# Optimization experiments

Measured on AMD Instinct MI355X. Metric: run time of the kernel, lower is better.

Reference implementation:

```python
import math
import jax, jax.numpy as jnp
import numpy as np

D_MODEL = 256
NUM_FEATURES = 512  # 2 * d_model (module default)
BATCH, SEQ = 4, 4096
EPS = 1e-6
INPUT_SCALE = 0.25  # keeps exp(xW/sqrt(d) - ||x||^2/2) numerically meaningful


def _make_projection(key):
    # Orthogonal random features: ceil(M/d)=2 QR blocks, then sqrt(|gauss|) row scaling.
    k1, k2, k3 = jax.random.split(key, 3)
    q1, _ = jnp.linalg.qr(jax.random.normal(k1, (D_MODEL, D_MODEL), jnp.float32))
    q2, _ = jnp.linalg.qr(jax.random.normal(k2, (D_MODEL, D_MODEL), jnp.float32))
    proj = jnp.concatenate([q1, q2], axis=1)[:, :NUM_FEATURES]  # (d, M)
    scaling = jnp.sqrt(jnp.abs(jax.random.normal(k3, (D_MODEL, 1), jnp.float32)))
    return proj * scaling


def setup_inputs() -> dict:
    key = jax.random.key(0)
    kq, kk, kv, kp = jax.random.split(key, 4)
    shape = (BATCH, SEQ, D_MODEL)
    return {
        "query": jax.random.normal(kq, shape, jnp.float32) * INPUT_SCALE,
        "key": jax.random.normal(kk, shape, jnp.float32) * INPUT_SCALE,
        "value": jax.random.normal(kv, shape, jnp.float32) * INPUT_SCALE,
        "projection": _make_projection(kp),  # (d_model, num_features) buffer
    }


def _phi(x, projection):
    # phi(x) = exp(xW/sqrt(d) - ||x||^2/2) / sqrt(M)
    d = x.shape[-1]
    m = projection.shape[-1]
    proj = jnp.matmul(x, projection) / math.sqrt(d)  # (B, L, M)
    sq = 0.5 * jnp.sum(x * x, axis=-1, keepdims=True)  # (B, L, 1)
    return jnp.exp(proj - sq) / math.sqrt(m)


def reference(query, key, value, projection):
    qp = _phi(query, projection)  # (B, L, M)
    kp = _phi(key, projection)    # (B, L, M)
    B, L, M = qp.shape
    D = value.shape[-1]

    # Causal linear attention: running KV-state scan, O(B*M*D) state
    # (same math as cumsum of k' (outer) v, without materializing (B,L,M,D)).
    def step(carry, inp):
        kv_state, k_state = carry  # (B,M,D), (B,M)
        q_t, k_t, v_t = inp        # (B,M), (B,M), (B,D)
        kv_state = kv_state + k_t[:, :, None] * v_t[:, None, :]
        k_state = k_state + k_t
        num = jnp.einsum('bm,bmd->bd', q_t, kv_state)
        den = jnp.einsum('bm,bm->b', q_t, k_state)[:, None] + EPS
        return (kv_state, k_state), num / den

    init = (jnp.zeros((B, M, D), qp.dtype), jnp.zeros((B, M), qp.dtype))
    xs = (jnp.swapaxes(qp, 0, 1), jnp.swapaxes(kp, 0, 1), jnp.swapaxes(value, 0, 1))
    _, out = jax.lax.scan(step, init, xs)  # (L, B, D)
    return jnp.swapaxes(out, 0, 1)  # (B, L, D)
```

## Files before the change

### kernel.cpp

```cpp
#include <hip/hip_runtime.h>

#define B_ 4
#define L_ 4096
#define D_ 256
#define M_ 512
#define C_ 256
#define NC_ 16
#define NG_ (B_*NC_)
#define EPS_ 1e-6f
#define RSQRT_D_ 0.0625f
#define RSQRT_M_ 0.044194173824159216f

typedef __attribute__((ext_vector_type(8))) short short8;
typedef __attribute__((ext_vector_type(4))) short short4v;
typedef __attribute__((ext_vector_type(4))) float floatx4;

__device__ __forceinline__ short f2b(float f) {
  union { float f; unsigned u; } c; c.f = f;
  unsigned r = c.u + 0x7fffu + ((c.u >> 16) & 1u);
  return (short)(r >> 16);
}
__device__ __forceinline__ float b2f(short s) {
  union { unsigned u; float f; } c; c.u = ((unsigned)(unsigned short)s) << 16;
  return c.f;
}

#define OFF_SB   0u
#define OFF_WT   16777216u
#define OFF_QP   17039360u
#define OFF_KP   33816576u
#define OFF_KPT  50593792u
#define OFF_VT   67371008u
#define OFF_AM   75759616u
#define OFF_PB   84148224u
#define OFF_ZP   100925440u

__device__ __forceinline__ void mfma_tile_gemm(
    const short* __restrict__ Ag, int lda,
    const short* __restrict__ Bg, int ldb,
    int K, short* sA, short* sB, floatx4 acc[4][4])
{
  const int tid  = threadIdx.x;
  const int lane = tid & 63;
  const int wave = tid >> 6;
  const int wm = wave >> 1, wn = wave & 1;
  const int q = lane >> 4, ml = lane & 15;

  short8 pa[4], pb[4];
  #pragma unroll
  for (int it = 0; it < 4; ++it) {
    int ci = tid + 256 * it;
    int m = ci >> 3, k8 = ci & 7;
    pa[it] = *(const short8*)(Ag + (size_t)m * lda + k8 * 8);
    pb[it] = *(const short8*)(Bg + (size_t)m * ldb + k8 * 8);
  }
  for (int k0 = 0; k0 < K; k0 += 64) {
    #pragma unroll
    for (int it = 0; it < 4; ++it) {
      int ci = tid + 256 * it;
      int m = ci >> 3, k8 = ci & 7;
      int dst = (k8 >> 2) * 512 + (m >> 4) * 64 + (k8 & 3) * 16 + ((m & 15) ^ k8);
      *(short8*)(sA + dst * 8) = pa[it];
      *(short8*)(sB + dst * 8) = pb[it];
    }
    if (k0 + 64 < K) {
      #pragma unroll
      for (int it = 0; it < 4; ++it) {
        int ci = tid + 256 * it;
        int m = ci >> 3, k8 = ci & 7;
        pa[it] = *(const short8*)(Ag + (size_t)m * lda + k0 + 64 + k8 * 8);
        pb[it] = *(const short8*)(Bg + (size_t)m * ldb + k0 + 64 + k8 * 8);
      }
    }
    __syncthreads();
    #pragma unroll
    for (int ks = 0; ks < 2; ++ks) {
      short8 a[4], b[4];
      int k8 = ks * 4 + q;
      #pragma unroll
      for (int i = 0; i < 4; ++i) {
        int ca = ks * 512 + (wm * 4 + i) * 64 + q * 16 + (ml ^ k8);
        a[i] = *(const short8*)(sA + ca * 8);
        int cb = ks * 512 + (wn * 4 + i) * 64 + q * 16 + (ml ^ k8);
        b[i] = *(const short8*)(sB + cb * 8);
      }
      #pragma unroll
      for (int i = 0; i < 4; ++i)
        #pragma unroll
        for (int j = 0; j < 4; ++j)
          acc[i][j] = __builtin_amdgcn_mfma_f32_16x16x32_bf16(a[i], b[j], acc[i][j], 0, 0, 0);
    }
    __syncthreads();
  }
}

__global__ __launch_bounds__(256) void transpose_cvt_kernel(
    const float* __restrict__ v, const float* __restrict__ W,
    short* __restrict__ vT, short* __restrict__ Wt)
{
  const int z = blockIdx.z;
  const float* src; short* dst; int ld_in, ld_out;
  if (z < NG_) {
    if (blockIdx.x >= 4) return;
    src = v + (size_t)z * (C_*D_) + (size_t)blockIdx.y * 64 * D_ + blockIdx.x * 64;
    dst = vT + (size_t)z * (D_*C_) + (size_t)blockIdx.x * 64 * C_ + blockIdx.y * 64;
    ld_in = D_; ld_out = C_;
  } else {
    src = W + (size_t)blockIdx.y * 64 * M_ + blockIdx.x * 64;
    dst = Wt + (size_t)blockIdx.x * 64 * D_ + blockIdx.y * 64;
    ld_in = M_; ld_out = D_;
  }
  __shared__ short sm[64 * 65];
  const int tid = threadIdx.x;
  #pragma unroll
  for (int it = 0; it < 4; ++it) {
    int ci = tid + 256 * it;
    int row = ci >> 4, c4 = ci & 15;
    float4 x = *(const float4*)(src + (size_t)row * ld_in + c4 * 4);
    sm[(c4 * 4 + 0) * 65 + row] = f2b(x.x);
    sm[(c4 * 4 + 1) * 65 + row] = f2b(x.y);
    sm[(c4 * 4 + 2) * 65 + row] = f2b(x.z);
    sm[(c4 * 4 + 3) * 65 + row] = f2b(x.w);
  }
  __syncthreads();
  #pragma unroll
  for (int it = 0; it < 2; ++it) {
    int ci = tid + 256 * it;
    int dr = ci >> 3, t8 = ci & 7;
    short8 o;
    #pragma unroll
    for (int u = 0; u < 8; ++u) o[u] = sm[dr * 65 + t8 * 8 + u];
    *(short8*)(dst + (size_t)dr * ld_out + t8 * 8) = o;
  }
}

__global__ __launch_bounds__(512) void phi_mfma_kernel(
    const float* __restrict__ qin, const float* __restrict__ kin,
    const short* __restrict__ Wt,
    short* __restrict__ qp, short* __restrict__ kp, short* __restrict__ kpT,
    float* __restrict__ ZP)
{
  const bool is_k = (blockIdx.z == 1);
  const float* X = is_k ? kin : qin;
  short* outP = is_k ? kp : qp;
  const int idl = blockIdx.x + 2 * blockIdx.y;
  const int row0 = ((idl & 7) + 8 * (idl >> 4)) * 128;
  const int col0 = ((idl >> 3) & 1) * 256;
  __shared__ short smem[34816];
  __shared__ float zsb[512];
  __shared__ float sqs[128];
  short* sA = smem;
  short* sB = smem + 8192;
  const int tid = threadIdx.x, lane = tid & 63, wave = tid >> 6;
  const int wm = wave >> 2, wn = wave & 3, q = lane >> 4, ml = lane & 15;
  const int c8 = tid & 7, r8 = tid >> 3;
  floatx4 acc[4][4];
  #pragma unroll
  for (int i = 0; i < 4; ++i)
    #pragma unroll
    for (int j = 0; j < 4; ++j) acc[i][j] = (floatx4){0.f,0.f,0.f,0.f};

  float4 px0[2], px1[2];
  #pragma unroll
  for (int it = 0; it < 2; ++it) {
    const float* src = X + (size_t)(row0 + r8 + 64 * it) * D_ + c8 * 8;
    px0[it] = *(const float4*)src;
    px1[it] = *(const float4*)(src + 4);
  }
  float ssq[2] = {0.f, 0.f};
  for (int k0 = 0; k0 < D_; k0 += 64) {
    #pragma unroll
    for (int it = 0; it < 2; ++it) {
      int m = r8 + 64 * it;
      float4 x0 = px0[it], x1 = px1[it];
      short8 vv;
      vv[0] = f2b(x0.x); vv[1] = f2b(x0.y); vv[2] = f2b(x0.z); vv[3] = f2b(x0.w);
      vv[4] = f2b(x1.x); vv[5] = f2b(x1.y); vv[6] = f2b(x1.z); vv[7] = f2b(x1.w);
      ssq[it] += x0.x*x0.x + x0.y*x0.y + x0.z*x0.z + x0.w*x0.w
               + x1.x*x1.x + x1.y*x1.y + x1.z*x1.z + x1.w*x1.w;
      *(short8*)(sA + (c8 * 128 + (m ^ c8)) * 8) = vv;
    }
    #pragma unroll
    for (int it = 0; it < 4; ++it) {
      int mm = r8 + 64 * it;
      short8 wb = *(const short8*)(Wt + (size_t)(col0 + mm) * D_ + k0 + c8 * 8);
      *(short8*)(sB + (c8 * 256 + (mm ^ c8)) * 8) = wb;
    }
    if (k0 + 64 < D_) {
      #pragma unroll
      for (int it = 0; it < 2; ++it) {
        const float* src = X + (size_t)(row0 + r8 + 64 * it) * D_ + k0 + 64 + c8 * 8;
        px0[it] = *(const float4*)src;
        px1[it] = *(const float4*)(src + 4);
      }
    }
    __syncthreads();
    #pragma unroll
    for (int ks = 0; ks < 2; ++ks) {
      short8 a[4], b[4];
      int kk = ks * 4 + q;
      #pragma unroll
      for (int i = 0; i < 4; ++i) {
        int ra = (wm * 64 + i * 16 + ml) ^ kk;
        a[i] = *(const short8*)(sA + (kk * 128 + ra) * 8);
        int rb = (wn * 64 + i * 16 + ml) ^ kk;
        b[i] = *(const short8*)(sB + (kk * 256 + rb) * 8);
      }
      #pragma unroll
      for (int i = 0; i < 4; ++i)
        #pragma unroll
        for (int j = 0; j < 4; ++j)
          acc[i][j] = __builtin_amdgcn_mfma_f32_16x16x32_bf16(a[i], b[j], acc[i][j], 0, 0, 0);
    }
    __syncthreads();
  }
  #pragma unroll
  for (int o = 1; o < 8; o <<= 1)
    #pragma unroll
    for (int it = 0; it < 2; ++it) ssq[it] += __shfl_xor(ssq[it], o);
  if (c8 == 0) {
    sqs[r8] = 0.5f * ssq[0];
    sqs[r8 + 64] = 0.5f * ssq[1];
  }
  __syncthreads();

  if (!is_k) {
    #pragma unroll
    for (int i = 0; i < 4; ++i) {
      int rl = wm * 64 + i * 16 + q * 4;
      float sqv[4];
      #pragma unroll
      for (int r = 0; r < 4; ++r) sqv[r] = sqs[rl + r];
      #pragma unroll
      for (int j = 0; j < 4; ++j) {
        int cl = wn * 64 + j * 16 + ml;
        #pragma unroll
        for (int r = 0; r < 4; ++r) {
          float pv = __expf(fmaf(acc[i][j][r], RSQRT_D_, -sqv[r])) * RSQRT_M_;
          smem[(size_t)(rl + r) * 264 + cl] = f2b(pv);
        }
      }
    }
    __syncthreads();
    #pragma unroll
    for (int it = 0; it < 8; ++it) {
      int idx = tid + 512 * it;
      int row = idx >> 5, cc8 = idx & 31;
      short8 vv = *(const short8*)(smem + (size_t)row * 264 + cc8 * 8);
      *(short8*)(outP + (size_t)(row0 + row) * M_ + col0 + cc8 * 8) = vv;
    }
  } else {
    float csum[4] = {0.f, 0.f, 0.f, 0.f};
    #pragma unroll
    for (int i = 0; i < 4; ++i) {
      int rl = wm * 64 + i * 16 + q * 4;
      float sqv[4];
      #pragma unroll
      for (int r = 0; r < 4; ++r) sqv[r] = sqs[rl + r];
      #pragma unroll
      for (int j = 0; j < 4; ++j) {
        int cl = wn * 64 + j * 16 + ml;
        short4v tb;
        #pragma unroll
        for (int r = 0; r < 4; ++r) {
          float pv = __expf(fmaf(acc[i][j][r], RSQRT_D_, -sqv[r])) * RSQRT_M_;
          short bv = f2b(pv);
          outP[(size_t)(row0 + rl + r) * M_ + col0 + cl] = bv;
          tb[r] = bv;
          csum[j] += b2f(bv);
        }
        *(short4v*)(smem + (size_t)cl * 136 + rl) = tb;
      }
    }
    #pragma unroll
    for (int j = 0; j < 4; ++j) {
      csum[j] += __shfl_xor(csum[j], 16);
      csum[j] += __shfl_xor(csum[j], 32);
    }
    if (lane < 16) {
      #pragma unroll
      for (int j = 0; j < 4; ++j)
        zsb[wm * 256 + wn * 64 + j * 16 + ml] = csum[j];
    }
    __syncthreads();
    int g = row0 >> 8, tb0 = row0 & 255;
    #pragma unroll
    for (int it = 0; it < 8; ++it) {
      int ci = tid + 512 * it;
      int t8 = ci & 15, cc = ci >> 4;
      short8 vv = *(const short8*)(smem + (size_t)cc * 136 + t8 * 8);
      *(short8*)(kpT + (size_t)g * (M_*C_) + (size_t)(col0 + cc) * C_ + tb0 + t8 * 8) = vv;
    }
    if (tid < 256) {
      float s = zsb[tid] + zsb[256 + tid];
      int p = (row0 >> 7) & 1;
      ZP[((size_t)g * 2 + p) * M_ + col0 + tid] = s;
    }
  }
}

__global__ __launch_bounds__(256) void mega_kernel(
    const short* __restrict__ vT, const short* __restrict__ kpT,
    const short* __restrict__ qp, const short* __restrict__ kp,
    short* __restrict__ Sb, short* __restrict__ Am)
{
  const int id = blockIdx.x + 4 * blockIdx.y + 12 * blockIdx.z;
  const int t12 = id >> 3;
  const int g  = (id & 7) + 8 * (t12 / 12);
  const int inner = t12 % 12;
  const int bx = inner & 3, by = inner >> 2;
  __shared__ short smem[17408];
  const int tid = threadIdx.x;

  floatx4 acc[4][4];
  #pragma unroll
  for (int i = 0; i < 4; ++i)
    #pragma unroll
    for (int j = 0; j < 4; ++j) acc[i][j] = (floatx4){0.f,0.f,0.f,0.f};
  const int lane = tid & 63, wave = tid >> 6;
  const int wm = wave >> 1, wn = wave & 1, q = lane >> 4, ln = lane & 15;

  if (by < 2) {
    const int m0 = bx * 128, d0 = by * 128;
    mfma_tile_gemm(vT + (size_t)g * (D_*C_) + (size_t)d0 * C_, C_,
                   kpT + (size_t)g * (M_*C_) + (size_t)m0 * C_, C_, C_,
                   smem, smem + 8192, acc);
    #pragma unroll
    for (int i = 0; i < 4; ++i) {
      int lr = wm * 64 + i * 16 + q * 4;
      #pragma unroll
      for (int j = 0; j < 4; ++j) {
        int lc = wn * 64 + j * 16 + ln;
        #pragma unroll
        for (int r = 0; r < 4; ++r)
          smem[(size_t)(lr + r) * 136 + lc] = f2b(acc[i][j][r]);
      }
    }
    __syncthreads();
    #pragma unroll
    for (int it = 0; it < 8; ++it) {
      int idx = tid + 256 * it;
      int row = idx >> 4, c8 = idx & 15;
      short8 vv = *(const short8*)(smem + (size_t)row * 136 + c8 * 8);
      *(short8*)(Sb + ((size_t)g * D_ + d0 + row) * M_ + m0 + c8 * 8) = vv;
    }
  } else {
    const int tt0 = (bx >> 1) * 128, tp0 = (bx & 1) * 128;
    short* Ag = Am + (size_t)g * (C_*C_);
    if (tp0 > tt0) {
      short8 z8 = 0;
      #pragma unroll
      for (int it = 0; it < 8; ++it) {
        int ci = tid + 256 * it;
        int row = ci >> 4, c8 = ci & 15;
        *(short8*)(Ag + (size_t)(tt0 + row) * C_ + tp0 + c8 * 8) = z8;
      }
      return;
    }
    const size_t cb = (size_t)g * C_;
    mfma_tile_gemm(qp + (cb + tt0) * M_, M_, kp + (cb + tp0) * M_, M_, M_,
                   smem, smem + 8192, acc);
    #pragma unroll
    for (int i = 0; i < 4; ++i) {
      int lr = wm * 64 + i * 16 + q * 4;
      #pragma unroll
      for (int j = 0; j < 4; ++j) {
        int lc = wn * 64 + j * 16 + ln;
        #pragma unroll
        for (int r = 0; r < 4; ++r) {
          short bv = ((tp0 + lc) <= (tt0 + lr + r)) ? f2b(acc[i][j][r]) : (short)0;
          smem[(size_t)(lr + r) * 136 + lc] = bv;
        }
      }
    }
    __syncthreads();
    #pragma unroll
    for (int it = 0; it < 8; ++it) {
      int idx = tid + 256 * it;
      int row = idx >> 4, c8 = idx & 15;
      short8 vv = *(const short8*)(smem + (size_t)row * 136 + c8 * 8);
      *(short8*)(Ag + (size_t)(tt0 + row) * C_ + tp0 + c8 * 8) = vv;
    }
  }
}

__global__ __launch_bounds__(256) void prefixS_kernel(
    const short* __restrict__ Sb, short* __restrict__ Pb)
{
  int j = blockIdx.x * 256 + threadIdx.x;
  int b = j >> 14, e8 = j & 16383;
  size_t base = ((size_t)b * NC_) * 131072 + (size_t)e8 * 8;
  short8 t[NC_];
  #pragma unroll
  for (int i = 0; i < NC_; ++i)
    t[i] = *(const short8*)(Sb + base + (size_t)i * 131072);
  float run[8] = {0.f,0.f,0.f,0.f,0.f,0.f,0.f,0.f};
  #pragma unroll
  for (int i = 0; i < NC_; ++i) {
    short8 o;
    #pragma unroll
    for (int u = 0; u < 8; ++u) { o[u] = f2b(run[u]); run[u] += b2f(t[i][u]); }
    *(short8*)(Pb + base + (size_t)i * 131072) = o;
  }
}

__global__ __launch_bounds__(256) void out_mfma_kernel(
    const short* __restrict__ qp, const short* __restrict__ Pb,
    const short* __restrict__ Am, const short* __restrict__ vT,
    const float* __restrict__ ZP, float* __restrict__ out)
{
  const int id = blockIdx.x + 2 * blockIdx.y + 8 * blockIdx.z;
  const int g  = (id & 7) + 8 * (id >> 6);
  const int inner = (id >> 3) & 7;
  const int d0 = (inner & 1) * 128, tt0 = (inner >> 1) * 64;
  __shared__ short smem[16896];
  __shared__ float zbuf[512];
  __shared__ float dbuf[64];
  short* sA = smem; short* sB = smem + 4096;
  const int tid = threadIdx.x, lane = tid & 63, wave = tid >> 6;
  const int wm = wave >> 1, wn = wave & 1, q = lane >> 4, ml = lane & 15;
  const int r8 = tid >> 3;

  {
    int b = g >> 4, gi = g & 15;
    float s0 = 0.f, s1 = 0.f;
    const float* zp0 = ZP + (size_t)(b * NC_) * 2 * M_;
    for (int i = 0; i < gi; ++i) {
      const float* r = zp0 + (size_t)i * 2 * M_;
      s0 += r[tid] + r[M_ + tid];
      s1 += r[tid + 256] + r[M_ + tid + 256];
    }
    zbuf[tid] = s0; zbuf[tid + 256] = s1;
    if (tid < 64) dbuf[tid] = 0.f;
  }
  __syncthreads();

  floatx4 acc[2][4];
  #pragma unroll
  for (int i = 0; i < 2; ++i)
    #pragma unroll
    for (int j = 0; j < 4; ++j) acc[i][j] = (floatx4){0.f,0.f,0.f,0.f};

  {
    const short* Ag = qp + ((size_t)g * C_ + tt0) * M_;
    const short* Bg = Pb + (size_t)g * (D_*M_) + (size_t)d0 * M_;
    float dp[2] = {0.f, 0.f};
    short8 pa[2], pb[4];
    #pragma unroll
    for (int it = 0; it < 2; ++it) {
      int ci = tid + 256 * it;
      int m = ci >> 3, k8 = ci & 7;
      pa[it] = *(const short8*)(Ag + (size_t)m * M_ + k8 * 8);
    }
    #pragma unroll
    for (int it = 0; it < 4; ++it) {
      int ci = tid + 256 * it;
      int m = ci >> 3, k8 = ci & 7;
      pb[it] = *(const short8*)(Bg + (size_t)m * M_ + k8 * 8);
    }
    for (int k0 = 0; k0 < M_; k0 += 64) {
      #pragma unroll
      for (int it = 0; it < 2; ++it) {
        int ci = tid + 256 * it;
        int m = ci >> 3, k8 = ci & 7;
        int dst = (k8 >> 2) * 256 + (m >> 4) * 64 + (k8 & 3) * 16 + ((m & 15) ^ k8);
        *(short8*)(sA + dst * 8) = pa[it];
        const float* zz = zbuf + k0 + k8 * 8;
        float d = 0.f;
        #pragma unroll
        for (int u = 0; u < 8; ++u) d = fmaf(b2f(pa[it][u]), zz[u], d);
        dp[it] += d;
      }
      #pragma unroll
      for (int it = 0; it < 4; ++it) {
        int ci = tid + 256 * it;
        int m = ci >> 3, k8 = ci & 7;
        int dst = (k8 >> 2) * 512 + (m >> 4) * 64 + (k8 & 3) * 16 + ((m & 15) ^ k8);
        *(short8*)(sB + dst * 8) = pb[it];
      }
      if (k0 + 64 < M_) {
        #pragma unroll
        for (int it = 0; it < 2; ++it) {
          int ci = tid + 256 * it;
          int m = ci >> 3, k8 = ci & 7;
          pa[it] = *(const short8*)(Ag + (size_t)m * M_ + k0 + 64 + k8 * 8);
        }
        #pragma unroll
        for (int it = 0; it < 4; ++it) {
          int ci = tid + 256 * it;
          int m = ci >> 3, k8 = ci & 7;
          pb[it] = *(const short8*)(Bg + (size_t)m * M_ + k0 + 64 + k8 * 8);
        }
      }
      __syncthreads();
      #pragma unroll
      for (int ks = 0; ks < 2; ++ks) {
        short8 a[2], b[4];
        int k8 = ks * 4 + q;
        #pragma unroll
        for (int i = 0; i < 2; ++i) {
          int ca = ks * 256 + (wm * 2 + i) * 64 + q * 16 + (ml ^ k8);
          a[i] = *(const short8*)(sA + ca * 8);
        }
        #pragma unroll
        for (int j = 0; j < 4; ++j) {
          int cb = ks * 512 + (wn * 4 + j) * 64 + q * 16 + (ml ^ k8);
          b[j] = *(const short8*)(sB + cb * 8);
        }
        #pragma unroll
        for (int i = 0; i < 2; ++i)
          #pragma unroll
          for (int j = 0; j < 4; ++j)
            acc[i][j] = __builtin_amdgcn_mfma_f32_16x16x32_bf16(a[i], b[j], acc[i][j], 0, 0, 0);
      }
      __syncthreads();
    }
    #pragma unroll
    for (int o = 1; o < 8; o <<= 1)
      #pragma unroll
      for (int it = 0; it < 2; ++it) dp[it] += __shfl_xor(dp[it], o);
    if ((tid & 7) == 0) {
      #pragma unroll
      for (int it = 0; it < 2; ++it) dbuf[r8 + 32 * it] += dp[it];
    }
  }

  {
    const short* Ag = Am + ((size_t)g * C_ + tt0) * C_;
    const short* Bg = vT + (size_t)g * (D_*C_) + (size_t)d0 * C_;
    float dp[2] = {0.f, 0.f};
    short8 pa[2], pb[4];
    #pragma unroll
    for (int it = 0; it < 2; ++it) {
      int ci = tid + 256 * it;
      int m = ci >> 3, k8 = ci & 7;
      pa[it] = *(const short8*)(Ag + (size_t)m * C_ + k8 * 8);
    }
    #pragma unroll
    for (int it = 0; it < 4; ++it) {
      int ci = tid + 256 * it;
      int m = ci >> 3, k8 = ci & 7;
      pb[it] = *(const short8*)(Bg + (size_t)m * C_ + k8 * 8);
    }
    for (int k0 = 0; k0 < C_; k0 += 64) {
      #pragma unroll
      for (int it = 0; it < 2; ++it) {
        int ci = tid + 256 * it;
        int m = ci >> 3, k8 = ci & 7;
        int dst = (k8 >> 2) * 256 + (m >> 4) * 64 + (k8 & 3) * 16 + ((m & 15) ^ k8);
        *(short8*)(sA + dst * 8) = pa[it];
        float d = 0.f;
        #pragma unroll
        for (int u = 0; u < 8; ++u) d += b2f(pa[it][u]);
        dp[it] += d;
      }
      #pragma unroll
      for (int it = 0; it < 4; ++it) {
        int ci = tid + 256 * it;
        int m = ci >> 3, k8 = ci & 7;
        int dst = (k8 >> 2) * 512 + (m >> 4) * 64 + (k8 & 3) * 16 + ((m & 15) ^ k8);
        *(short8*)(sB + dst * 8) = pb[it];
      }
      if (k0 + 64 < C_) {
        #pragma unroll
        for (int it = 0; it < 2; ++it) {
          int ci = tid + 256 * it;
          int m = ci >> 3, k8 = ci & 7;
          pa[it] = *(const short8*)(Ag + (size_t)m * C_ + k0 + 64 + k8 * 8);
        }
        #pragma unroll
        for (int it = 0; it < 4; ++it) {
          int ci = tid + 256 * it;
          int m = ci >> 3, k8 = ci & 7;
          pb[it] = *(const short8*)(Bg + (size_t)m * C_ + k0 + 64 + k8 * 8);
        }
      }
      __syncthreads();
      #pragma unroll
      for (int ks = 0; ks < 2; ++ks) {
        short8 a[2], b[4];
        int k8 = ks * 4 + q;
        #pragma unroll
        for (int i = 0; i < 2; ++i) {
          int ca = ks * 256 + (wm * 2 + i) * 64 + q * 16 + (ml ^ k8);
          a[i] = *(const short8*)(sA + ca * 8);
        }
        #pragma unroll
        for (int j = 0; j < 4; ++j) {
          int cb = ks * 512 + (wn * 4 + j) * 64 + q * 16 + (ml ^ k8);
          b[j] = *(const short8*)(sB + cb * 8);
        }
        #pragma unroll
        for (int i = 0; i < 2; ++i)
          #pragma unroll
          for (int j = 0; j < 4; ++j)
            acc[i][j] = __builtin_amdgcn_mfma_f32_16x16x32_bf16(a[i], b[j], acc[i][j], 0, 0, 0);
      }
      __syncthreads();
    }
    #pragma unroll
    for (int o = 1; o < 8; o <<= 1)
      #pragma unroll
      for (int it = 0; it < 2; ++it) dp[it] += __shfl_xor(dp[it], o);
    if ((tid & 7) == 0) {
      #pragma unroll
      for (int it = 0; it < 2; ++it) dbuf[r8 + 32 * it] += dp[it];
    }
  }
  __syncthreads();

  float* smF = (float*)smem;
  #pragma unroll
  for (int i = 0; i < 2; ++i) {
    int lr = wm * 32 + i * 16 + q * 4;
    #pragma unroll
    for (int r = 0; r < 4; ++r) {
      float rc = 1.0f / (dbuf[lr + r] + EPS_);
      #pragma unroll
      for (int j = 0; j < 4; ++j) {
        int lc = wn * 64 + j * 16 + ml;
        smF[(size_t)(lr + r) * 132 + lc] = acc[i][j][r] * rc;
      }
    }
  }
  __syncthreads();
  #pragma unroll
  for (int it = 0; it < 8; ++it) {
    int idx = tid + 256 * it;
    int row = idx >> 5, c4 = idx & 31;
    float4 val = *(const float4*)(smF + (size_t)row * 132 + c4 * 4);
    *(float4*)(out + (size_t)(g * C_ + tt0 + row) * D_ + d0 + c4 * 4) = val;
  }
}

extern "C" void kernel_launch(void* const* d_in, const int* in_sizes, int n_in,
                              void* d_out, int out_size, void* d_ws, size_t ws_size,
                              hipStream_t stream) {
  const float* q = (const float*)d_in[0];
  const float* k = (const float*)d_in[1];
  const float* v = (const float*)d_in[2];
  const float* W = (const float*)d_in[3];
  float* out = (float*)d_out;
  char* ws = (char*)d_ws;

  short* Sb  = (short*)(ws + OFF_SB);
  short* Wt  = (short*)(ws + OFF_WT);
  short* qp  = (short*)(ws + OFF_QP);
  short* kp  = (short*)(ws + OFF_KP);
  short* kpT = (short*)(ws + OFF_KPT);
  short* vT  = (short*)(ws + OFF_VT);
  short* Am  = (short*)(ws + OFF_AM);
  short* Pb  = (short*)(ws + OFF_PB);
  float* ZP  = (float*)(ws + OFF_ZP);

  transpose_cvt_kernel<<<dim3(8, 4, NG_ + 1), 256, 0, stream>>>(v, W, vT, Wt);
  phi_mfma_kernel<<<dim3(2, 128, 2), 512, 0, stream>>>(q, k, Wt, qp, kp, kpT, ZP);
  mega_kernel<<<dim3(4, 3, NG_), 256, 0, stream>>>(vT, kpT, qp, kp, Sb, Am);
  prefixS_kernel<<<(B_*D_*M_)/2048, 256, 0, stream>>>(Sb, Pb);
  out_mfma_kernel<<<dim3(2, 4, NG_), 256, 0, stream>>>(qp, Pb, Am, vT, ZP, out);
}
```

Measured before the change: 156.5 us.

## Stage GEMM tiles with direct global-to-LDS async loads instead of register prefetch

Replaces the register-staged prefetch (global load to VGPRs, then LDS store) in several GEMM loops with global_load_lds 16-byte direct copies. Per-thread source addresses are permuted so that the contiguous LDS destination reproduces the existing XOR-swizzled layout. This removes the VGPR staging and the LDS write instructions, but also drops the software prefetch overlap: each k-step now issues its loads and waits at a barrier before computing. The row-sum and dot-product side computations now reread the A tile from LDS.

```diff
diff --git a/kernel.cpp b/kernel.cpp
--- a/kernel.cpp
+++ b/kernel.cpp
@@ -25,6 +25,12 @@
   return c.f;
 }
 
+__device__ __forceinline__ void async_copy16(const short* g, short* l) {
+  __builtin_amdgcn_global_load_lds(
+      (const __attribute__((address_space(1))) void*)(g),
+      (__attribute__((address_space(3))) void*)(l), 16, 0, 0);
+}
+
 #define OFF_SB   0u
 #define OFF_WT   16777216u
 #define OFF_QP   17039360u
@@ -46,31 +52,21 @@
   const int wm = wave >> 1, wn = wave & 1;
   const int q = lane >> 4, ml = lane & 15;
 
-  short8 pa[4], pb[4];
+  int mloc[4], koff[4];
   #pragma unroll
   for (int it = 0; it < 4; ++it) {
-    int ci = tid + 256 * it;
-    int m = ci >> 3, k8 = ci & 7;
-    pa[it] = *(const short8*)(Ag + (size_t)m * lda + k8 * 8);
-    pb[it] = *(const short8*)(Bg + (size_t)m * ldb + k8 * 8);
+    int s = tid + 256 * it;
+    int x = s & 15, l = (s >> 4) & 3, M = (s >> 6) & 7, h = s >> 9;
+    int k8 = 4 * h + l;
+    mloc[it] = M * 16 + (x ^ k8);
+    koff[it] = k8 * 8;
   }
   for (int k0 = 0; k0 < K; k0 += 64) {
     #pragma unroll
     for (int it = 0; it < 4; ++it) {
-      int ci = tid + 256 * it;
-      int m = ci >> 3, k8 = ci & 7;
-      int dst = (k8 >> 2) * 512 + (m >> 4) * 64 + (k8 & 3) * 16 + ((m & 15) ^ k8);
-      *(short8*)(sA + dst * 8) = pa[it];
-      *(short8*)(sB + dst * 8) = pb[it];
-    }
-    if (k0 + 64 < K) {
-      #pragma unroll
-      for (int it = 0; it < 4; ++it) {
-        int ci = tid + 256 * it;
-        int m = ci >> 3, k8 = ci & 7;
-        pa[it] = *(const short8*)(Ag + (size_t)m * lda + k0 + 64 + k8 * 8);
-        pb[it] = *(const short8*)(Bg + (size_t)m * ldb + k0 + 64 + k8 * 8);
-      }
+      int s = tid + 256 * it;
+      async_copy16(Ag + (size_t)mloc[it] * lda + k0 + koff[it], sA + s * 8);
+      async_copy16(Bg + (size_t)mloc[it] * ldb + k0 + koff[it], sB + s * 8);
     }
     __syncthreads();
     #pragma unroll
@@ -160,6 +156,15 @@
     #pragma unroll
     for (int j = 0; j < 4; ++j) acc[i][j] = (floatx4){0.f,0.f,0.f,0.f};
 
+  int wmm[4], wc8[4];
+  #pragma unroll
+  for (int it = 0; it < 4; ++it) {
+    int s = tid + 512 * it;
+    int cc = s >> 8;
+    wmm[it] = (s & 255) ^ cc;
+    wc8[it] = cc;
+  }
+
   float4 px0[2], px1[2];
   #pragma unroll
   for (int it = 0; it < 2; ++it) {
@@ -169,6 +174,11 @@
   }
   float ssq[2] = {0.f, 0.f};
   for (int k0 = 0; k0 < D_; k0 += 64) {
+    #pragma unroll
+    for (int it = 0; it < 4; ++it) {
+      int s = tid + 512 * it;
+      async_copy16(Wt + (size_t)(col0 + wmm[it]) * D_ + k0 + wc8[it] * 8, sB + s * 8);
+    }
     #pragma unroll
     for (int it = 0; it < 2; ++it) {
       int m = r8 + 64 * it;
@@ -179,12 +189,6 @@
       ssq[it] += x0.x*x0.x + x0.y*x0.y + x0.z*x0.z + x0.w*x0.w
                + x1.x*x1.x + x1.y*x1.y + x1.z*x1.z + x1.w*x1.w;
       *(short8*)(sA + (c8 * 128 + (m ^ c8)) * 8) = vv;
-    }
-    #pragma unroll
-    for (int it = 0; it < 4; ++it) {
-      int mm = r8 + 64 * it;
-      short8 wb = *(const short8*)(Wt + (size_t)(col0 + mm) * D_ + k0 + c8 * 8);
-      *(short8*)(sB + (c8 * 256 + (mm ^ c8)) * 8) = wb;
     }
     if (k0 + 64 < D_) {
       #pragma unroll
@@ -435,6 +439,22 @@
   }
   __syncthreads();
 
+  int mA[2], kA[2], mB[4], kB[4];
+  #pragma unroll
+  for (int it = 0; it < 2; ++it) {
+    int s = tid + 256 * it;
+    int x = s & 15, l = (s >> 4) & 3, M = (s >> 6) & 3, h = s >> 8;
+    int k8 = 4 * h + l;
+    mA[it] = M * 16 + (x ^ k8); kA[it] = k8 * 8;
+  }
+  #pragma unroll
+  for (int it = 0; it < 4; ++it) {
+    int s = tid + 256 * it;
+    int x = s & 15, l = (s >> 4) & 3, M = (s >> 6) & 7, h = s >> 9;
+    int k8 = 4 * h + l;
+    mB[it] = M * 16 + (x ^ k8); kB[it] = k8 * 8;
+  }
+
   floatx4 acc[2][4];
   #pragma unroll
   for (int i = 0; i < 2; ++i)
@@ -445,54 +465,26 @@
     const short* Ag = qp + ((size_t)g * C_ + tt0) * M_;
     const short* Bg = Pb + (size_t)g * (D_*M_) + (size_t)d0 * M_;
     float dp[2] = {0.f, 0.f};
-    short8 pa[2], pb[4];
-    #pragma unroll
-    for (int it = 0; it < 2; ++it) {
-      int ci = tid + 256 * it;
-      int m = ci >> 3, k8 = ci & 7;
-      pa[it] = *(const short8*)(Ag + (size_t)m * M_ + k8 * 8);
-    }
-    #pragma unroll
-    for (int it = 0; it < 4; ++it) {
-      int ci = tid + 256 * it;
-      int m = ci >> 3, k8 = ci & 7;
-      pb[it] = *(const short8*)(Bg + (size_t)m * M_ + k8 * 8);
-    }
     for (int k0 = 0; k0 < M_; k0 += 64) {
+      #pragma unroll
+      for (int it = 0; it < 2; ++it)
+        async_copy16(Ag + (size_t)mA[it] * M_ + k0 + kA[it], sA + (tid + 256 * it) * 8);
+      #pragma unroll
+      for (int it = 0; it < 4; ++it)
+        async_copy16(Bg + (size_t)mB[it] * M_ + k0 + kB[it], sB + (tid + 256 * it) * 8);
+      __syncthreads();
       #pragma unroll
       for (int it = 0; it < 2; ++it) {
         int ci = tid + 256 * it;
         int m = ci >> 3, k8 = ci & 7;
         int dst = (k8 >> 2) * 256 + (m >> 4) * 64 + (k8 & 3) * 16 + ((m & 15) ^ k8);
-        *(short8*)(sA + dst * 8) = pa[it];
+        short8 pa = *(const short8*)(sA + dst * 8);
         const float* zz = zbuf + k0 + k8 * 8;
         float d = 0.f;
         #pragma unroll
-        for (int u = 0; u < 8; ++u) d = fmaf(b2f(pa[it][u]), zz[u], d);
+        for (int u = 0; u < 8; ++u) d = fmaf(b2f(pa[u]), zz[u], d);
         dp[it] += d;
       }
-      #pragma unroll
-      for (int it = 0; it < 4; ++it) {
-        int ci = tid + 256 * it;
-        int m = ci >> 3, k8 = ci & 7;
-        int dst = (k8 >> 2) * 512 + (m >> 4) * 64 + (k8 & 3) * 16 + ((m & 15) ^ k8);
-        *(short8*)(sB + dst * 8) = pb[it];
-      }
-      if (k0 + 64 < M_) {
-        #pragma unroll
-        for (int it = 0; it < 2; ++it) {
-          int ci = tid + 256 * it;
-          int m = ci >> 3, k8 = ci & 7;
-          pa[it] = *(const short8*)(Ag + (size_t)m * M_ + k0 + 64 + k8 * 8);
-        }
-        #pragma unroll
-        for (int it = 0; it < 4; ++it) {
-          int ci = tid + 256 * it;
-          int m = ci >> 3, k8 = ci & 7;
-          pb[it] = *(const short8*)(Bg + (size_t)m * M_ + k0 + 64 + k8 * 8);
-        }
-      }
-      __syncthreads();
       #pragma unroll
       for (int ks = 0; ks < 2; ++ks) {
         short8 a[2], b[4];
@@ -529,53 +521,25 @@
     const short* Ag = Am + ((size_t)g * C_ + tt0) * C_;
     const short* Bg = vT + (size_t)g * (D_*C_) + (size_t)d0 * C_;
     float dp[2] = {0.f, 0.f};
-    short8 pa[2], pb[4];
-    #pragma unroll
-    for (int it = 0; it < 2; ++it) {
-      int ci = tid + 256 * it;
-      int m = ci >> 3, k8 = ci & 7;
-      pa[it] = *(const short8*)(Ag + (size_t)m * C_ + k8 * 8);
-    }
-    #pragma unroll
-    for (int it = 0; it < 4; ++it) {
-      int ci = tid + 256 * it;
-      int m = ci >> 3, k8 = ci & 7;
-      pb[it] = *(const short8*)(Bg + (size_t)m * C_ + k8 * 8);
-    }
     for (int k0 = 0; k0 < C_; k0 += 64) {
+      #pragma unroll
+      for (int it = 0; it < 2; ++it)
+        async_copy16(Ag + (size_t)mA[it] * C_ + k0 + kA[it], sA + (tid + 256 * it) * 8);
+      #pragma unroll
+      for (int it = 0; it < 4; ++it)
+        async_copy16(Bg + (size_t)mB[it] * C_ + k0 + kB[it], sB + (tid + 256 * it) * 8);
+      __syncthreads();
       #pragma unroll
       for (int it = 0; it < 2; ++it) {
         int ci = tid + 256 * it;
         int m = ci >> 3, k8 = ci & 7;
         int dst = (k8 >> 2) * 256 + (m >> 4) * 64 + (k8 & 3) * 16 + ((m & 15) ^ k8);
-        *(short8*)(sA + dst * 8) = pa[it];
+        short8 pa = *(const short8*)(sA + dst * 8);
         float d = 0.f;
         #pragma unroll
-        for (int u = 0; u < 8; ++u) d += b2f(pa[it][u]);
+        for (int u = 0; u < 8; ++u) d += b2f(pa[u]);
         dp[it] += d;
       }
-      #pragma unroll
-      for (int it = 0; it < 4; ++it) {
-        int ci = tid + 256 * it;
-        int m = ci >> 3, k8 = ci & 7;
-        int dst = (k8 >> 2) * 512 + (m >> 4) * 64 + (k8 & 3) * 16 + ((m & 15) ^ k8);
-        *(short8*)(sB + dst * 8) = pb[it];
-      }
-      if (k0 + 64 < C_) {
-        #pragma unroll
-        for (int it = 0; it < 2; ++it) {
-          int ci = tid + 256 * it;
-          int m = ci >> 3, k8 = ci & 7;
-          pa[it] = *(const short8*)(Ag + (size_t)m * C_ + k0 + 64 + k8 * 8);
-        }
-        #pragma unroll
-        for (int it = 0; it < 4; ++it) {
-          int ci = tid + 256 * it;
-          int m = ci >> 3, k8 = ci & 7;
-          pb[it] = *(const short8*)(Bg + (size_t)m * C_ + k0 + 64 + k8 * 8);
-        }
-      }
-      __syncthreads();
       #pragma unroll
       for (int ks = 0; ks < 2; ++ks) {
         short8 a[2], b[4];
```

Measured after the change: 175.6 us. 12.2% more time.

## Use direct global-to-LDS async loads in tile GEMM and precompute z prefix sums

Applied to the files above, without the earlier changes.

The shared MFMA tile GEMM now stages A/B tiles with global_load_lds direct-to-LDS copies in an unswizzled layout, replacing the register-staged prefetch and XOR-swizzled stores. Separately, the per-chunk prefix sum of key-feature totals (ZP) is computed once by extra blocks in prefixS_kernel into ZPX, which reuses the Wt workspace slot. out_mfma_kernel then reads that instead of looping over previous chunks. The GEMM change drops the prefetch overlap and swizzle, so it risks LDS bank conflicts and exposed load latency, and the Wt region must no longer be needed by the time prefixS runs.

```diff
diff --git a/kernel.cpp b/kernel.cpp
--- a/kernel.cpp
+++ b/kernel.cpp
@@ -25,6 +25,12 @@
   return c.f;
 }
 
+__device__ __forceinline__ void async_copy16(const short* g, short* l) {
+  __builtin_amdgcn_global_load_lds(
+      (const __attribute__((address_space(1))) void*)(g),
+      (__attribute__((address_space(3))) void*)(l), 16, 0, 0);
+}
+
 #define OFF_SB   0u
 #define OFF_WT   16777216u
 #define OFF_QP   17039360u
@@ -46,31 +52,13 @@
   const int wm = wave >> 1, wn = wave & 1;
   const int q = lane >> 4, ml = lane & 15;
 
-  short8 pa[4], pb[4];
-  #pragma unroll
-  for (int it = 0; it < 4; ++it) {
-    int ci = tid + 256 * it;
-    int m = ci >> 3, k8 = ci & 7;
-    pa[it] = *(const short8*)(Ag + (size_t)m * lda + k8 * 8);
-    pb[it] = *(const short8*)(Bg + (size_t)m * ldb + k8 * 8);
-  }
   for (int k0 = 0; k0 < K; k0 += 64) {
     #pragma unroll
     for (int it = 0; it < 4; ++it) {
-      int ci = tid + 256 * it;
-      int m = ci >> 3, k8 = ci & 7;
-      int dst = (k8 >> 2) * 512 + (m >> 4) * 64 + (k8 & 3) * 16 + ((m & 15) ^ k8);
-      *(short8*)(sA + dst * 8) = pa[it];
-      *(short8*)(sB + dst * 8) = pb[it];
-    }
-    if (k0 + 64 < K) {
-      #pragma unroll
-      for (int it = 0; it < 4; ++it) {
-        int ci = tid + 256 * it;
-        int m = ci >> 3, k8 = ci & 7;
-        pa[it] = *(const short8*)(Ag + (size_t)m * lda + k0 + 64 + k8 * 8);
-        pb[it] = *(const short8*)(Bg + (size_t)m * ldb + k0 + 64 + k8 * 8);
-      }
+      int s = tid + 256 * it;
+      int m = s >> 3, k8 = s & 7;
+      async_copy16(Ag + (size_t)m * lda + k0 + k8 * 8, sA + s * 8);
+      async_copy16(Bg + (size_t)m * ldb + k0 + k8 * 8, sB + s * 8);
     }
     __syncthreads();
     #pragma unroll
@@ -79,10 +67,10 @@
       int k8 = ks * 4 + q;
       #pragma unroll
       for (int i = 0; i < 4; ++i) {
-        int ca = ks * 512 + (wm * 4 + i) * 64 + q * 16 + (ml ^ k8);
-        a[i] = *(const short8*)(sA + ca * 8);
-        int cb = ks * 512 + (wn * 4 + i) * 64 + q * 16 + (ml ^ k8);
-        b[i] = *(const short8*)(sB + cb * 8);
+        int ra = wm * 64 + i * 16 + ml;
+        a[i] = *(const short8*)(sA + (ra * 8 + k8) * 8);
+        int rb = wn * 64 + i * 16 + ml;
+        b[i] = *(const short8*)(sB + (rb * 8 + k8) * 8);
       }
       #pragma unroll
       for (int i = 0; i < 4; ++i)
@@ -385,8 +373,21 @@
 }
 
 __global__ __launch_bounds__(256) void prefixS_kernel(
-    const short* __restrict__ Sb, short* __restrict__ Pb)
+    const short* __restrict__ Sb, short* __restrict__ Pb,
+    const float* __restrict__ ZP, float* __restrict__ ZPX)
 {
+  if (blockIdx.x >= 256) {
+    int idx = (blockIdx.x - 256) * 256 + threadIdx.x;
+    int b = idx >> 9, m = idx & 511;
+    float run = 0.f;
+    #pragma unroll
+    for (int i = 0; i < NC_; ++i) {
+      int g = b * NC_ + i;
+      ZPX[(size_t)g * M_ + m] = run;
+      run += ZP[((size_t)g * 2 + 0) * M_ + m] + ZP[((size_t)g * 2 + 1) * M_ + m];
+    }
+    return;
+  }
   int j = blockIdx.x * 256 + threadIdx.x;
   int b = j >> 14, e8 = j & 16383;
   size_t base = ((size_t)b * NC_) * 131072 + (size_t)e8 * 8;
@@ -407,7 +408,7 @@
 __global__ __launch_bounds__(256) void out_mfma_kernel(
     const short* __restrict__ qp, const short* __restrict__ Pb,
     const short* __restrict__ Am, const short* __restrict__ vT,
-    const float* __restrict__ ZP, float* __restrict__ out)
+    const float* __restrict__ ZPX, float* __restrict__ out)
 {
   const int id = blockIdx.x + 2 * blockIdx.y + 8 * blockIdx.z;
   const int g  = (id & 7) + 8 * (id >> 6);
@@ -422,15 +423,8 @@
   const int r8 = tid >> 3;
 
   {
-    int b = g >> 4, gi = g & 15;
-    float s0 = 0.f, s1 = 0.f;
-    const float* zp0 = ZP + (size_t)(b * NC_) * 2 * M_;
-    for (int i = 0; i < gi; ++i) {
-      const float* r = zp0 + (size_t)i * 2 * M_;
-      s0 += r[tid] + r[M_ + tid];
-      s1 += r[tid + 256] + r[M_ + tid + 256];
-    }
-    zbuf[tid] = s0; zbuf[tid + 256] = s1;
+    zbuf[tid]       = ZPX[(size_t)g * M_ + tid];
+    zbuf[tid + 256] = ZPX[(size_t)g * M_ + 256 + tid];
     if (tid < 64) dbuf[tid] = 0.f;
   }
   __syncthreads();
@@ -652,10 +646,11 @@
   short* Am  = (short*)(ws + OFF_AM);
   short* Pb  = (short*)(ws + OFF_PB);
   float* ZP  = (float*)(ws + OFF_ZP);
+  float* ZPX = (float*)(ws + OFF_WT);
 
   transpose_cvt_kernel<<<dim3(8, 4, NG_ + 1), 256, 0, stream>>>(v, W, vT, Wt);
   phi_mfma_kernel<<<dim3(2, 128, 2), 512, 0, stream>>>(q, k, Wt, qp, kp, kpT, ZP);
   mega_kernel<<<dim3(4, 3, NG_), 256, 0, stream>>>(vT, kpT, qp, kp, Sb, Am);
-  prefixS_kernel<<<(B_*D_*M_)/2048, 256, 0, stream>>>(Sb, Pb);
-  out_mfma_kernel<<<dim3(2, 4, NG_), 256, 0, stream>>>(qp, Pb, Am, vT, ZP, out);
-}
+  prefixS_kernel<<<264, 256, 0, stream>>>(Sb, Pb, ZP, ZPX);
+  out_mfma_kernel<<<dim3(2, 4, NG_), 256, 0, stream>>>(qp, Pb, Am, vT, ZPX, out);
+}
```

Result: no change. 156.9 us, median of 2 (+0.2%).
